# Performance work log

Hardware: AMD Instinct MI355X
Metric: run time of the kernel (lower is better)

The kernel has to match this reference:

```python
import jax, jax.numpy as jnp
import numpy as np

N_NODES = 100000
N_EDGES = 640000
IN_CH = 128
HID = 128


def setup_inputs() -> dict:
    key = jax.random.key(0)
    k1, k2, k3, k4, k5 = jax.random.split(key, 5)
    z = jax.random.normal(k1, (N_NODES, IN_CH), dtype=jnp.float32)
    edge_index = jax.random.randint(k2, (2, N_EDGES), 0, N_NODES, dtype=jnp.int64)
    # Linear layers: stored as [in, out] for x @ W + b
    s1 = 1.0 / np.sqrt(2 * IN_CH)
    W1 = jax.random.uniform(k3, (2 * IN_CH, HID), minval=-s1, maxval=s1, dtype=jnp.float32)
    b1 = jnp.zeros((HID,), dtype=jnp.float32)
    s2 = 1.0 / np.sqrt(HID)
    W2 = jax.random.uniform(k4, (HID, 1), minval=-s2, maxval=s2, dtype=jnp.float32)
    b2 = jnp.zeros((1,), dtype=jnp.float32)
    return {"z": z, "edge_index": edge_index, "W1": W1, "b1": b1, "W2": W2, "b2": b2}


def reference(z, edge_index, W1, b1, W2, b2):
    # gather source/destination node embeddings and concat -> [E, 2*C]
    h = jnp.concatenate([z[edge_index[0]], z[edge_index[1]]], axis=-1)
    h = jax.nn.relu(h @ W1 + b1)  # [E, HID]; Dropout(0.2) is identity in eval
    out = h @ W2 + b2             # [E, 1]
    return out.squeeze(-1)        # [E]
```

## Files before the change

### kernel.cpp

```cpp
#include <hip/hip_runtime.h>
#include <hip/hip_bf16.h>

typedef short bf16x8 __attribute__((ext_vector_type(8)));
typedef float f32x4  __attribute__((ext_vector_type(4)));
typedef unsigned short u16;

static __device__ __forceinline__ u16 f2bf(float f) {
    unsigned u = __float_as_uint(f);
    u += 0x7FFFu + ((u >> 16) & 1u);
    return (u16)(u >> 16);
}
static __device__ __forceinline__ float bf2f(u16 b) {
    return __uint_as_float(((unsigned)b) << 16);
}
static __device__ __forceinline__ unsigned pack2(float lo, float hi) {
    return (unsigned)f2bf(lo) | ((unsigned)f2bf(hi) << 16);
}

__global__ void prep_w(const float* __restrict__ W1, u16* __restrict__ Wl) {
    int idx = blockIdx.x * 256 + threadIdx.x;
    if (idx >= 256 * 128) return;
    int r = idx >> 7;
    int q = idx & 127;
    int k = (r < 128) ? r : (r - 128);
    int c = (r < 128) ? q : (q + 128);
    Wl[c * 128 + k] = f2bf(W1[idx]);
}

#define BM 128
__global__ __launch_bounds__(256, 2) void node_gemm(
    const float* __restrict__ z,
    const u16*   __restrict__ Wl,
    u16*         __restrict__ PQ,
    int M)
{
    __shared__ char As[BM * 256];
    const int tid  = threadIdx.x;
    const int lane = tid & 63;
    const int wave = tid >> 6;
    const int m0   = blockIdx.x * BM;

    #pragma unroll
    for (int i = 0; i < (BM * 32) / 256; ++i) {
        int ci  = tid + i * 256;
        int row = ci >> 5;
        int c4  = ci & 31;
        float4 v = make_float4(0.f, 0.f, 0.f, 0.f);
        if (m0 + row < M)
            v = *(const float4*)(z + (size_t)(m0 + row) * 128 + c4 * 4);
        ushort4 b;
        b.x = f2bf(v.x); b.y = f2bf(v.y); b.z = f2bf(v.z); b.w = f2bf(v.w);
        int byte = row * 256 + ((c4 * 8) ^ ((row & 7) << 4));
        *(ushort4*)(As + byte) = b;
    }
    __syncthreads();

    f32x4 acc[8][4];
    #pragma unroll
    for (int mf = 0; mf < 8; ++mf)
        #pragma unroll
        for (int ci = 0; ci < 4; ++ci)
            acc[mf][ci] = (f32x4){0.f, 0.f, 0.f, 0.f};

    const int g  = lane >> 4;
    const int ln = lane & 15;
    const int c0 = wave * 64;

    #pragma unroll
    for (int ks = 0; ks < 4; ++ks) {
        bf16x8 a[4];
        #pragma unroll
        for (int ci = 0; ci < 4; ++ci)
            a[ci] = *(const bf16x8*)(Wl + (c0 + ci * 16 + ln) * 128 + ks * 32 + g * 8);
        #pragma unroll
        for (int mf = 0; mf < 8; ++mf) {
            int row  = mf * 16 + ln;
            int byte = row * 256 + ((ks * 64 + g * 16) ^ ((row & 7) << 4));
            bf16x8 b = *(const bf16x8*)(As + byte);
            #pragma unroll
            for (int ci = 0; ci < 4; ++ci)
                acc[mf][ci] = __builtin_amdgcn_mfma_f32_16x16x32_bf16(
                    a[ci], b, acc[mf][ci], 0, 0, 0);
        }
    }

    #pragma unroll
    for (int mf = 0; mf < 8; ++mf) {
        int node = m0 + mf * 16 + ln;
        if (node < M) {
            #pragma unroll
            for (int ci = 0; ci < 4; ++ci) {
                uint2 w;
                w.x = pack2(acc[mf][ci][0], acc[mf][ci][1]);
                w.y = pack2(acc[mf][ci][2], acc[mf][ci][3]);
                *(uint2*)(PQ + (size_t)node * 256 + c0 + ci * 16 + g * 4) = w;
            }
        }
    }
}

__global__ __launch_bounds__(256) void edge_mlp(
    const int* __restrict__ ei,
    const u16* __restrict__ PQ,
    const float* __restrict__ b1,
    const float* __restrict__ W2,
    const float* __restrict__ b2,
    float* __restrict__ out,
    int E)
{
    int gid  = blockIdx.x * 256 + threadIdx.x;
    int e0   = (gid >> 4) * 2;
    int sub  = gid & 15;
    if (e0 >= E) return;
    bool two = (e0 + 1) < E;

    int2 ss, dd;
    if (two) {
        ss = *(const int2*)(ei + e0);
        dd = *(const int2*)(ei + E + e0);
    } else {
        ss.x = ei[e0];     ss.y = ss.x;
        dd.x = ei[E + e0]; dd.y = dd.x;
    }

    uint4 p0 = *(const uint4*)(PQ + (size_t)ss.x * 256 + sub * 8);
    uint4 q0 = *(const uint4*)(PQ + (size_t)dd.x * 256 + 128 + sub * 8);
    uint4 p1 = *(const uint4*)(PQ + (size_t)ss.y * 256 + sub * 8);
    uint4 q1 = *(const uint4*)(PQ + (size_t)dd.y * 256 + 128 + sub * 8);

    float4 b1a = *(const float4*)(b1 + sub * 8);
    float4 b1b = *(const float4*)(b1 + sub * 8 + 4);
    float4 w2a = *(const float4*)(W2 + sub * 8);
    float4 w2b = *(const float4*)(W2 + sub * 8 + 4);
    float bb[8] = {b1a.x, b1a.y, b1a.z, b1a.w, b1b.x, b1b.y, b1b.z, b1b.w};
    float ww[8] = {w2a.x, w2a.y, w2a.z, w2a.w, w2b.x, w2b.y, w2b.z, w2b.w};

    const u16* p0u = (const u16*)&p0;
    const u16* q0u = (const u16*)&q0;
    const u16* p1u = (const u16*)&p1;
    const u16* q1u = (const u16*)&q1;

    float acc0 = 0.f, acc1 = 0.f;
    #pragma unroll
    for (int j = 0; j < 8; ++j) {
        float h0 = bf2f(p0u[j]) + bf2f(q0u[j]) + bb[j];
        float h1 = bf2f(p1u[j]) + bf2f(q1u[j]) + bb[j];
        acc0 = fmaf(fmaxf(h0, 0.f), ww[j], acc0);
        acc1 = fmaf(fmaxf(h1, 0.f), ww[j], acc1);
    }
    #pragma unroll
    for (int m = 1; m < 16; m <<= 1) {
        acc0 += __shfl_xor(acc0, m);
        acc1 += __shfl_xor(acc1, m);
    }

    if (sub == 0) {
        float bias = b2[0];
        if (two) {
            float2 o = make_float2(acc0 + bias, acc1 + bias);
            *(float2*)(out + e0) = o;
        } else {
            out[e0] = acc0 + bias;
        }
    }
}

extern "C" void kernel_launch(void* const* d_in, const int* in_sizes, int n_in,
                              void* d_out, int out_size, void* d_ws, size_t ws_size,
                              hipStream_t stream) {
    const float* z  = (const float*)d_in[0];
    const int*   ei = (const int*)d_in[1];
    const float* W1 = (const float*)d_in[2];
    const float* b1 = (const float*)d_in[3];
    const float* W2 = (const float*)d_in[4];
    const float* b2 = (const float*)d_in[5];
    float* out = (float*)d_out;

    const int M = in_sizes[0] / 128;
    const int E = in_sizes[1] / 2;

    u16* Wl = (u16*)d_ws;
    u16* PQ = (u16*)((char*)d_ws + 65536);

    hipLaunchKernelGGL(prep_w, dim3(128), dim3(256), 0, stream, W1, Wl);

    int gb = (M + BM - 1) / BM;
    hipLaunchKernelGGL(node_gemm, dim3(gb), dim3(256), 0, stream, z, Wl, PQ, M);

    int eb = (E * 8 + 255) / 256;
    hipLaunchKernelGGL(edge_mlp, dim3(eb), dim3(256), 0, stream,
                       ei, PQ, b1, W2, b2, out, E);
}
```

Measured before the change: 88.40 us.

## Persistent double-buffered node GEMM, fold b1 into PQ, 4 edges per group

The node GEMM becomes a persistent kernel capped at 512 blocks with 64-row tiles. Each block prefetches the next tile of z into registers and a second LDS buffer while it computes the current tile, which is meant to hide global load latency. The b1 bias is added to the P half during the GEMM epilogue, so the edge kernel no longer loads or adds it. The edge kernel now handles four edges per 16-lane group, putting more independent gathers in flight. The cost is higher register pressure and extra bf16 rounding from adding the bias before the PQ store.

```diff
diff --git a/kernel.cpp b/kernel.cpp
--- a/kernel.cpp
+++ b/kernel.cpp
@@ -27,140 +27,201 @@
     Wl[c * 128 + k] = f2bf(W1[idx]);
 }
 
-#define BM 128
+#define BM 64
 __global__ __launch_bounds__(256, 2) void node_gemm(
     const float* __restrict__ z,
     const u16*   __restrict__ Wl,
+    const float* __restrict__ b1,
     u16*         __restrict__ PQ,
-    int M)
+    int M, int ntiles)
 {
-    __shared__ char As[BM * 256];
+    __shared__ char As[2][BM * 256];
     const int tid  = threadIdx.x;
     const int lane = tid & 63;
     const int wave = tid >> 6;
-    const int m0   = blockIdx.x * BM;
-
+    const int g    = lane >> 4;
+    const int ln   = lane & 15;
+    const int c0   = wave * 64;
+
+    int t = blockIdx.x;
+    if (t >= ntiles) return;
+
+    float4 bias[4];
     #pragma unroll
-    for (int i = 0; i < (BM * 32) / 256; ++i) {
-        int ci  = tid + i * 256;
-        int row = ci >> 5;
-        int c4  = ci & 31;
-        float4 v = make_float4(0.f, 0.f, 0.f, 0.f);
-        if (m0 + row < M)
-            v = *(const float4*)(z + (size_t)(m0 + row) * 128 + c4 * 4);
-        ushort4 b;
-        b.x = f2bf(v.x); b.y = f2bf(v.y); b.z = f2bf(v.z); b.w = f2bf(v.w);
-        int byte = row * 256 + ((c4 * 8) ^ ((row & 7) << 4));
-        *(ushort4*)(As + byte) = b;
+    for (int ci = 0; ci < 4; ++ci) {
+        int col = c0 + ci * 16 + g * 4;
+        bias[ci] = (col < 128) ? *(const float4*)(b1 + col)
+                               : make_float4(0.f, 0.f, 0.f, 0.f);
+    }
+
+    float4 r[8];
+
+    {
+        int m0 = t * BM;
+        #pragma unroll
+        for (int i = 0; i < 8; ++i) {
+            int ci = tid + i * 256, row = ci >> 5, c4 = ci & 31;
+            r[i] = make_float4(0.f, 0.f, 0.f, 0.f);
+            if (m0 + row < M)
+                r[i] = *(const float4*)(z + (size_t)(m0 + row) * 128 + c4 * 4);
+        }
+        #pragma unroll
+        for (int i = 0; i < 8; ++i) {
+            int ci = tid + i * 256, row = ci >> 5, c4 = ci & 31;
+            ushort4 b;
+            b.x = f2bf(r[i].x); b.y = f2bf(r[i].y);
+            b.z = f2bf(r[i].z); b.w = f2bf(r[i].w);
+            *(ushort4*)(As[0] + row * 256 + ((c4 * 8) ^ ((row & 7) << 4))) = b;
+        }
     }
     __syncthreads();
 
-    f32x4 acc[8][4];
-    #pragma unroll
-    for (int mf = 0; mf < 8; ++mf)
-        #pragma unroll
-        for (int ci = 0; ci < 4; ++ci)
-            acc[mf][ci] = (f32x4){0.f, 0.f, 0.f, 0.f};
-
-    const int g  = lane >> 4;
-    const int ln = lane & 15;
-    const int c0 = wave * 64;
-
-    #pragma unroll
-    for (int ks = 0; ks < 4; ++ks) {
-        bf16x8 a[4];
-        #pragma unroll
-        for (int ci = 0; ci < 4; ++ci)
-            a[ci] = *(const bf16x8*)(Wl + (c0 + ci * 16 + ln) * 128 + ks * 32 + g * 8);
-        #pragma unroll
-        for (int mf = 0; mf < 8; ++mf) {
-            int row  = mf * 16 + ln;
-            int byte = row * 256 + ((ks * 64 + g * 16) ^ ((row & 7) << 4));
-            bf16x8 b = *(const bf16x8*)(As + byte);
+    int cur = 0;
+    while (true) {
+        int next = t + gridDim.x;
+        bool have = (next < ntiles);
+
+        if (have) {
+            int m0 = next * BM;
+            #pragma unroll
+            for (int i = 0; i < 8; ++i) {
+                int ci = tid + i * 256, row = ci >> 5, c4 = ci & 31;
+                r[i] = make_float4(0.f, 0.f, 0.f, 0.f);
+                if (m0 + row < M)
+                    r[i] = *(const float4*)(z + (size_t)(m0 + row) * 128 + c4 * 4);
+            }
+        }
+
+        f32x4 acc[4][4];
+        #pragma unroll
+        for (int mf = 0; mf < 4; ++mf)
             #pragma unroll
             for (int ci = 0; ci < 4; ++ci)
-                acc[mf][ci] = __builtin_amdgcn_mfma_f32_16x16x32_bf16(
-                    a[ci], b, acc[mf][ci], 0, 0, 0);
-        }
-    }
-
-    #pragma unroll
-    for (int mf = 0; mf < 8; ++mf) {
-        int node = m0 + mf * 16 + ln;
-        if (node < M) {
-            #pragma unroll
-            for (int ci = 0; ci < 4; ++ci) {
-                uint2 w;
-                w.x = pack2(acc[mf][ci][0], acc[mf][ci][1]);
-                w.y = pack2(acc[mf][ci][2], acc[mf][ci][3]);
-                *(uint2*)(PQ + (size_t)node * 256 + c0 + ci * 16 + g * 4) = w;
-            }
-        }
+                acc[mf][ci] = (f32x4){0.f, 0.f, 0.f, 0.f};
+
+        #pragma unroll
+        for (int ks = 0; ks < 4; ++ks) {
+            bf16x8 a[4];
+            #pragma unroll
+            for (int ci = 0; ci < 4; ++ci)
+                a[ci] = *(const bf16x8*)(Wl + (c0 + ci * 16 + ln) * 128 + ks * 32 + g * 8);
+            #pragma unroll
+            for (int mf = 0; mf < 4; ++mf) {
+                int row  = mf * 16 + ln;
+                int byte = row * 256 + ((ks * 64 + g * 16) ^ ((row & 7) << 4));
+                bf16x8 b = *(const bf16x8*)(As[cur] + byte);
+                #pragma unroll
+                for (int ci = 0; ci < 4; ++ci)
+                    acc[mf][ci] = __builtin_amdgcn_mfma_f32_16x16x32_bf16(
+                        a[ci], b, acc[mf][ci], 0, 0, 0);
+            }
+        }
+
+        if (have) {
+            #pragma unroll
+            for (int i = 0; i < 8; ++i) {
+                int ci = tid + i * 256, row = ci >> 5, c4 = ci & 31;
+                ushort4 b;
+                b.x = f2bf(r[i].x); b.y = f2bf(r[i].y);
+                b.z = f2bf(r[i].z); b.w = f2bf(r[i].w);
+                *(ushort4*)(As[cur ^ 1] + row * 256 + ((c4 * 8) ^ ((row & 7) << 4))) = b;
+            }
+        }
+
+        {
+            int m0 = t * BM;
+            #pragma unroll
+            for (int mf = 0; mf < 4; ++mf) {
+                int node = m0 + mf * 16 + ln;
+                if (node < M) {
+                    #pragma unroll
+                    for (int ci = 0; ci < 4; ++ci) {
+                        uint2 w;
+                        w.x = pack2(acc[mf][ci][0] + bias[ci].x,
+                                    acc[mf][ci][1] + bias[ci].y);
+                        w.y = pack2(acc[mf][ci][2] + bias[ci].z,
+                                    acc[mf][ci][3] + bias[ci].w);
+                        *(uint2*)(PQ + (size_t)node * 256 + c0 + ci * 16 + g * 4) = w;
+                    }
+                }
+            }
+        }
+
+        if (!have) break;
+        __syncthreads();
+        cur ^= 1;
+        t = next;
     }
 }
 
 __global__ __launch_bounds__(256) void edge_mlp(
     const int* __restrict__ ei,
     const u16* __restrict__ PQ,
-    const float* __restrict__ b1,
     const float* __restrict__ W2,
     const float* __restrict__ b2,
     float* __restrict__ out,
     int E)
 {
-    int gid  = blockIdx.x * 256 + threadIdx.x;
-    int e0   = (gid >> 4) * 2;
-    int sub  = gid & 15;
+    int gid = blockIdx.x * 256 + threadIdx.x;
+    int e0  = (gid >> 4) * 4;
+    int sub = gid & 15;
     if (e0 >= E) return;
-    bool two = (e0 + 1) < E;
-
-    int2 ss, dd;
-    if (two) {
-        ss = *(const int2*)(ei + e0);
-        dd = *(const int2*)(ei + E + e0);
-    } else {
-        ss.x = ei[e0];     ss.y = ss.x;
-        dd.x = ei[E + e0]; dd.y = dd.x;
-    }
-
-    uint4 p0 = *(const uint4*)(PQ + (size_t)ss.x * 256 + sub * 8);
-    uint4 q0 = *(const uint4*)(PQ + (size_t)dd.x * 256 + 128 + sub * 8);
-    uint4 p1 = *(const uint4*)(PQ + (size_t)ss.y * 256 + sub * 8);
-    uint4 q1 = *(const uint4*)(PQ + (size_t)dd.y * 256 + 128 + sub * 8);
-
-    float4 b1a = *(const float4*)(b1 + sub * 8);
-    float4 b1b = *(const float4*)(b1 + sub * 8 + 4);
+
     float4 w2a = *(const float4*)(W2 + sub * 8);
     float4 w2b = *(const float4*)(W2 + sub * 8 + 4);
-    float bb[8] = {b1a.x, b1a.y, b1a.z, b1a.w, b1b.x, b1b.y, b1b.z, b1b.w};
     float ww[8] = {w2a.x, w2a.y, w2a.z, w2a.w, w2b.x, w2b.y, w2b.z, w2b.w};
-
-    const u16* p0u = (const u16*)&p0;
-    const u16* q0u = (const u16*)&q0;
-    const u16* p1u = (const u16*)&p1;
-    const u16* q1u = (const u16*)&q1;
-
-    float acc0 = 0.f, acc1 = 0.f;
-    #pragma unroll
-    for (int j = 0; j < 8; ++j) {
-        float h0 = bf2f(p0u[j]) + bf2f(q0u[j]) + bb[j];
-        float h1 = bf2f(p1u[j]) + bf2f(q1u[j]) + bb[j];
-        acc0 = fmaf(fmaxf(h0, 0.f), ww[j], acc0);
-        acc1 = fmaf(fmaxf(h1, 0.f), ww[j], acc1);
-    }
-    #pragma unroll
-    for (int m = 1; m < 16; m <<= 1) {
-        acc0 += __shfl_xor(acc0, m);
-        acc1 += __shfl_xor(acc1, m);
-    }
-
-    if (sub == 0) {
-        float bias = b2[0];
-        if (two) {
-            float2 o = make_float2(acc0 + bias, acc1 + bias);
-            *(float2*)(out + e0) = o;
-        } else {
-            out[e0] = acc0 + bias;
+    float bias = b2[0];
+
+    if (e0 + 3 < E) {
+        int4 s = *(const int4*)(ei + e0);
+        int4 d = *(const int4*)(ei + E + e0);
+        uint4 p0 = *(const uint4*)(PQ + (size_t)s.x * 256 + sub * 8);
+        uint4 p1 = *(const uint4*)(PQ + (size_t)s.y * 256 + sub * 8);
+        uint4 p2 = *(const uint4*)(PQ + (size_t)s.z * 256 + sub * 8);
+        uint4 p3 = *(const uint4*)(PQ + (size_t)s.w * 256 + sub * 8);
+        uint4 q0 = *(const uint4*)(PQ + (size_t)d.x * 256 + 128 + sub * 8);
+        uint4 q1 = *(const uint4*)(PQ + (size_t)d.y * 256 + 128 + sub * 8);
+        uint4 q2 = *(const uint4*)(PQ + (size_t)d.z * 256 + 128 + sub * 8);
+        uint4 q3 = *(const uint4*)(PQ + (size_t)d.w * 256 + 128 + sub * 8);
+
+        float a0 = 0.f, a1 = 0.f, a2 = 0.f, a3 = 0.f;
+        const u16* pu0 = (const u16*)&p0; const u16* qu0 = (const u16*)&q0;
+        const u16* pu1 = (const u16*)&p1; const u16* qu1 = (const u16*)&q1;
+        const u16* pu2 = (const u16*)&p2; const u16* qu2 = (const u16*)&q2;
+        const u16* pu3 = (const u16*)&p3; const u16* qu3 = (const u16*)&q3;
+        #pragma unroll
+        for (int j = 0; j < 8; ++j) {
+            a0 = fmaf(fmaxf(bf2f(pu0[j]) + bf2f(qu0[j]), 0.f), ww[j], a0);
+            a1 = fmaf(fmaxf(bf2f(pu1[j]) + bf2f(qu1[j]), 0.f), ww[j], a1);
+            a2 = fmaf(fmaxf(bf2f(pu2[j]) + bf2f(qu2[j]), 0.f), ww[j], a2);
+            a3 = fmaf(fmaxf(bf2f(pu3[j]) + bf2f(qu3[j]), 0.f), ww[j], a3);
+        }
+        #pragma unroll
+        for (int m = 1; m < 16; m <<= 1) {
+            a0 += __shfl_xor(a0, m);
+            a1 += __shfl_xor(a1, m);
+            a2 += __shfl_xor(a2, m);
+            a3 += __shfl_xor(a3, m);
+        }
+        if (sub == 0) {
+            float4 o = make_float4(a0 + bias, a1 + bias, a2 + bias, a3 + bias);
+            *(float4*)(out + e0) = o;
+        }
+    } else {
+        for (int k = 0; k < 4; ++k) {
+            int e = e0 + k;
+            if (e >= E) break;
+            int sn = ei[e], dn = ei[E + e];
+            uint4 p = *(const uint4*)(PQ + (size_t)sn * 256 + sub * 8);
+            uint4 q = *(const uint4*)(PQ + (size_t)dn * 256 + 128 + sub * 8);
+            const u16* pu = (const u16*)&p; const u16* qu = (const u16*)&q;
+            float a = 0.f;
+            #pragma unroll
+            for (int j = 0; j < 8; ++j)
+                a = fmaf(fmaxf(bf2f(pu[j]) + bf2f(qu[j]), 0.f), ww[j], a);
+            #pragma unroll
+            for (int m = 1; m < 16; m <<= 1) a += __shfl_xor(a, m);
+            if (sub == 0) out[e] = a + bias;
         }
     }
 }
@@ -184,10 +245,12 @@
 
     hipLaunchKernelGGL(prep_w, dim3(128), dim3(256), 0, stream, W1, Wl);
 
-    int gb = (M + BM - 1) / BM;
-    hipLaunchKernelGGL(node_gemm, dim3(gb), dim3(256), 0, stream, z, Wl, PQ, M);
-
-    int eb = (E * 8 + 255) / 256;
+    int ntiles = (M + BM - 1) / BM;
+    int gb = ntiles < 512 ? ntiles : 512;
+    hipLaunchKernelGGL(node_gemm, dim3(gb), dim3(256), 0, stream,
+                       z, Wl, b1, PQ, M, ntiles);
+
+    int eb = ((E + 3) / 4 * 16 + 255) / 256;
     hipLaunchKernelGGL(edge_mlp, dim3(eb), dim3(256), 0, stream,
-                       ei, PQ, b1, W2, b2, out, E);
-}
+                       ei, PQ, W2, b2, out, E);
+}
```

New measurement: 80.97 us. -8.4%, faster.
